# Performance work log

Hardware: AMD Instinct MI355X
Metric: run time of the kernel (lower is better)

## Reference

```python
import jax, jax.numpy as jnp
import numpy as np

N_ENTITY = 100000
H_DIM = 512
N_ROWS = 262144
ALPHA = 0.5          # EMA rate for fast state
GATE_TH = 0.5        # gate_threshold buffer
GATE_SCALE = 5.0     # gate_scale buffer
LN_EPS = 1e-5


def setup_inputs() -> dict:
    key = jax.random.key(0)
    k1, k2, k3, k4, k5 = jax.random.split(key, 5)
    entity_emb = jax.random.normal(k1, (N_ROWS, H_DIM), dtype=jnp.float32)
    entity_ids = jax.random.randint(k2, (N_ROWS,), 0, N_ENTITY, dtype=jnp.int64)
    slow_state = 0.1 * jax.random.normal(k3, (N_ENTITY, H_DIM), dtype=jnp.float32)
    fast_state = 0.1 * jax.random.normal(k4, (N_ENTITY, H_DIM), dtype=jnp.float32)
    # torch nn.Linear(2h, h): weight shape (h, 2h), y = x @ W.T + b
    W = jax.random.normal(k5, (H_DIM, 2 * H_DIM), dtype=jnp.float32) * 0.02
    b = jnp.zeros((H_DIM,), dtype=jnp.float32)
    return {"entity_emb": entity_emb, "slow_state": slow_state,
            "fast_state": fast_state, "W": W, "b": b, "entity_ids": entity_ids}


def _layer_norm(x):
    mu = jnp.mean(x, axis=-1, keepdims=True)
    var = jnp.mean(jnp.square(x - mu), axis=-1, keepdims=True)
    return (x - mu) * jax.lax.rsqrt(var + LN_EPS)


def reference(entity_emb, slow_state, fast_state, W, b, entity_ids):
    # ---- fuse_with_state (gate path) ----
    state = slow_state[entity_ids]                                   # (N, h) gather
    is_active = (jnp.sum(jnp.abs(state), axis=-1, keepdims=True) > 1e-6).astype(entity_emb.dtype)
    h_state = _layer_norm(state)
    gate_in = jnp.concatenate([entity_emb, h_state], axis=-1)        # (N, 2h)
    z = jax.nn.sigmoid(gate_in @ W.T + b)                            # (N, h)
    fused = z * entity_emb + (1.0 - z) * h_state
    out = is_active * fused + (1.0 - is_active) * entity_emb

    # ---- writeback (no-grad in torch; scatter-reduce EMA + norm-gated slow update) ----
    ctx = jax.lax.stop_gradient(out)
    ids = entity_ids
    counts = jax.ops.segment_sum(jnp.ones((ctx.shape[0],), ctx.dtype), ids,
                                 num_segments=N_ENTITY)              # (E,)
    ctx_sum = jax.ops.segment_sum(ctx, ids, num_segments=N_ENTITY)   # (E, h)
    ctx_mean = ctx_sum / jnp.clip(counts, 1.0)[:, None]
    touched = (counts > 0)[:, None]
    new_fast_all = (1.0 - ALPHA) * fast_state + ALPHA * ctx_mean
    new_fast = jnp.where(touched, new_fast_all, fast_state)
    diff = new_fast - slow_state
    delta = jnp.linalg.norm(diff, axis=-1, keepdims=True)
    gate = jax.nn.sigmoid(GATE_SCALE * (delta - GATE_TH))
    new_slow = jnp.where(touched, slow_state + gate * diff, slow_state)
    return out, new_fast, new_slow
```

## Files before the change

### kernel.cpp

```cpp
#include <hip/hip_runtime.h>
#include <hip/hip_bf16.h>
#include <cstdint>

#define NROWS 262144
#define HDIM  512
#define NENT  100000
#define SCAN_NBLK ((NENT + 1023) / 1024)

typedef __attribute__((ext_vector_type(4))) float  f32x4;
typedef __attribute__((ext_vector_type(8))) short  bf16x8;
typedef __attribute__((ext_vector_type(4))) short  bf16x4;

static __device__ __forceinline__ unsigned short f2bf(float x) {
    unsigned u = __float_as_uint(x);
    u += 0x7FFF + ((u >> 16) & 1);
    return (unsigned short)(u >> 16);
}
static __device__ __forceinline__ float bf2f(unsigned short h) {
    return __uint_as_float(((unsigned)h) << 16);
}

__global__ void pack_w_kernel(const float* __restrict__ W,
                              unsigned short* __restrict__ WeP,
                              unsigned short* __restrict__ WsP) {
    int g    = blockIdx.x * 256 + threadIdx.x;
    int sel  = g >> 15;
    int gg   = g & 32767;
    int lane = gg & 63;
    int kt   = (gg >> 6) & 15;
    int nt   = gg >> 10;
    int col  = nt * 16 + (lane & 15);
    int k    = kt * 32 + ((lane >> 4) << 3) + sel * 512;
    const float* src = W + (size_t)col * 1024 + k;
    f32x4 v0 = *(const f32x4*)(src);
    f32x4 v1 = *(const f32x4*)(src + 4);
    bf16x8 ov;
#pragma unroll
    for (int i = 0; i < 4; ++i) {
        ov[i]     = (short)f2bf(v0[i]);
        ov[4 + i] = (short)f2bf(v1[i]);
    }
    unsigned short* dst = sel ? WsP : WeP;
    *(bf16x8*)(dst + (size_t)gg * 8) = ov;
}

__global__ __launch_bounds__(256) void zero_kernel(unsigned* __restrict__ p) {
    int i = blockIdx.x * 256 + threadIdx.x;
    if (i < NENT) p[i] = 0u;
}

__global__ __launch_bounds__(256) void count_kernel(const int* __restrict__ ids,
                                                    unsigned* __restrict__ counts) {
    int r = blockIdx.x * 256 + threadIdx.x;
    if (r < NROWS) atomicAdd(&counts[ids[r]], 1u);
}

__global__ __launch_bounds__(1024) void scan1_kernel(const unsigned* __restrict__ counts,
                                                     unsigned* __restrict__ off,
                                                     unsigned* __restrict__ bsums) {
    __shared__ unsigned tmp[1024];
    int i = blockIdx.x * 1024 + threadIdx.x;
    unsigned v = (i < NENT) ? counts[i] : 0u;
    tmp[threadIdx.x] = v;
    __syncthreads();
#pragma unroll
    for (int o = 1; o < 1024; o <<= 1) {
        unsigned a = (threadIdx.x >= o) ? tmp[threadIdx.x - o] : 0u;
        __syncthreads();
        tmp[threadIdx.x] += a;
        __syncthreads();
    }
    if (i < NENT) off[i] = tmp[threadIdx.x] - v;
    if (threadIdx.x == 1023) bsums[blockIdx.x] = tmp[1023];
}

__global__ void scan2_kernel(unsigned* __restrict__ bsums) {
    if (threadIdx.x == 0 && blockIdx.x == 0) {
        unsigned s = 0;
        for (int i = 0; i < SCAN_NBLK; ++i) { unsigned t = bsums[i]; bsums[i] = s; s += t; }
    }
}

__global__ __launch_bounds__(1024) void scan3_kernel(unsigned* __restrict__ off,
                                                     const unsigned* __restrict__ bsums,
                                                     unsigned* __restrict__ cursor) {
    int i = blockIdx.x * 1024 + threadIdx.x;
    if (i < NENT) {
        unsigned o = off[i] + bsums[blockIdx.x];
        off[i] = o;
        cursor[i] = o;
    }
    if (i == 0) off[NENT] = NROWS;
}

__global__ __launch_bounds__(256) void fill_kernel(const int* __restrict__ ids,
                                                   unsigned* __restrict__ cursor,
                                                   int* __restrict__ rowidx) {
    int r = blockIdx.x * 256 + threadIdx.x;
    if (r < NROWS) {
        unsigned p = atomicAdd(&cursor[ids[r]], 1u);
        rowidx[p] = r;
    }
}

__global__ __launch_bounds__(512, 4) void entity_kernel(
    const float* __restrict__ slow, const unsigned short* __restrict__ WsP,
    const float* __restrict__ bias, unsigned short* __restrict__ hB,
    unsigned short* __restrict__ GsB, float* __restrict__ actB)
{
    __shared__ unsigned short xLds[2048 * 8];
    __shared__ float muS[32], rsS[32], bS[512];

    const int t    = threadIdx.x;
    const int w    = t >> 6;
    const int lane = t & 63;
    const int brow = blockIdx.x * 32;

    if (t < 128) ((f32x4*)bS)[t] = ((const f32x4*)bias)[t];

    for (int rr = 0; rr < 4; ++rr) {
        int row = w * 4 + rr;
        int e   = brow + row;
        const float* sp = slow + (size_t)e * HDIM;
        f32x4 v0 = ((const f32x4*)sp)[lane * 2];
        f32x4 v1 = ((const f32x4*)sp)[lane * 2 + 1];
        float s = 0.f, s2 = 0.f, sa = 0.f;
#pragma unroll
        for (int i = 0; i < 4; ++i) {
            s  += v0[i] + v1[i];
            s2 += v0[i] * v0[i] + v1[i] * v1[i];
            sa += fabsf(v0[i]) + fabsf(v1[i]);
        }
#pragma unroll
        for (int m = 32; m >= 1; m >>= 1) {
            s  += __shfl_xor(s, m);
            s2 += __shfl_xor(s2, m);
            sa += __shfl_xor(sa, m);
        }
        if (lane == 0) {
            float mu  = s * (1.f / HDIM);
            float var = s2 * (1.f / HDIM) - mu * mu;
            muS[row] = mu;
            rsS[row] = rsqrtf(var + 1e-5f);
            actB[e]  = (sa > 1e-6f) ? 1.f : 0.f;
        }
    }
    __syncthreads();

#pragma unroll
    for (int i = 0; i < 4; ++i) {
        int s  = t + i * 512;
        int T  = s >> 6, ls = s & 63;
        int row = (T & 1) * 16 + (ls & 15);
        int k   = (T >> 1) * 32 + ((ls >> 4) << 3);
        const float* p = slow + (size_t)(brow + row) * HDIM + k;
        f32x4 x0 = *(const f32x4*)p, x1 = *(const f32x4*)(p + 4);
        float mu = muS[row], rs = rsS[row];
        bf16x8 av;
#pragma unroll
        for (int j = 0; j < 4; ++j) {
            av[j]     = (short)f2bf((x0[j] - mu) * rs);
            av[4 + j] = (short)f2bf((x1[j] - mu) * rs);
        }
        ((bf16x8*)xLds)[s] = av;
    }
    __syncthreads();

    f32x4 zero4 = {0.f, 0.f, 0.f, 0.f};
    f32x4 acc[2][4];
#pragma unroll
    for (int i = 0; i < 2; ++i)
#pragma unroll
        for (int j = 0; j < 4; ++j) acc[i][j] = zero4;

#define LOADW_A(dst, kt)                                                \
    {   _Pragma("unroll")                                               \
        for (int ct = 0; ct < 4; ++ct)                                  \
            dst[ct] = *(const bf16x8*)(WsP +                            \
                ((size_t)(((w * 4 + ct) * 16 + (kt)) * 64 + lane) << 3)); \
    }
#define LOADX_A(dst, kt)                                                \
    {   _Pragma("unroll")                                               \
        for (int rt = 0; rt < 2; ++rt)                                  \
            dst[rt] = ((const bf16x8*)xLds)[((kt) * 2 + rt) * 64 + lane]; \
    }
#define STEP(wf, xf)                                                    \
    {   _Pragma("unroll")                                               \
        for (int ct = 0; ct < 4; ++ct) {                                \
            acc[0][ct] = __builtin_amdgcn_mfma_f32_16x16x32_bf16(wf[ct], xf[0], acc[0][ct], 0, 0, 0); \
            acc[1][ct] = __builtin_amdgcn_mfma_f32_16x16x32_bf16(wf[ct], xf[1], acc[1][ct], 0, 0, 0); \
        }                                                               \
    }

    {
        bf16x8 wA[4], wB[4], xA[2], xB[2];
        LOADW_A(wA, 0); LOADX_A(xA, 0);
#pragma unroll
        for (int kt = 0; kt < 16; kt += 2) {
            if (kt + 1 < 16) { LOADW_A(wB, kt + 1); LOADX_A(xB, kt + 1); }
            STEP(wA, xA);
            if (kt + 2 < 16) { LOADW_A(wA, kt + 2); LOADX_A(xA, kt + 2); }
            if (kt + 1 < 16) STEP(wB, xB);
        }
    }
#undef LOADW_A
#undef LOADX_A

#pragma unroll
    for (int rt = 0; rt < 2; ++rt) {
        int e = brow + rt * 16 + (lane & 15);
#pragma unroll
        for (int ct = 0; ct < 4; ++ct) {
            int col0 = w * 64 + ct * 16 + ((lane >> 4) << 2);
            f32x4 bv = *(const f32x4*)&bS[col0];
            bf16x4 gv;
#pragma unroll
            for (int r = 0; r < 4; ++r) gv[r] = (short)f2bf(acc[rt][ct][r] + bv[r]);
            *(bf16x4*)(GsB + (size_t)e * HDIM + col0) = gv;
        }
    }
#pragma unroll
    for (int i = 0; i < 4; ++i) {
        int s  = t + i * 512;
        int T  = s >> 6, ls = s & 63;
        int row = (T & 1) * 16 + (ls & 15);
        int k   = (T >> 1) * 32 + ((ls >> 4) << 3);
        *(bf16x8*)(hB + (size_t)(brow + row) * HDIM + k) = ((const bf16x8*)xLds)[s];
    }
}

__global__ __launch_bounds__(1024, 4) void fuse_kernel(
    const float* __restrict__ emb, const unsigned short* __restrict__ WeP,
    const int* __restrict__ ids, const unsigned short* __restrict__ hB,
    const unsigned short* __restrict__ GsB, const float* __restrict__ actB,
    float* __restrict__ out)
{
    __shared__ unsigned short xLds[4096 * 8];
    __shared__ int idS[64];

    const int t    = threadIdx.x;
    const int w    = t >> 6;
    const int lane = t & 63;
    const int wm   = w >> 3;
    const int wn   = w & 7;
    const int brow = blockIdx.x * 64;

    if (t < 64) idS[t] = ids[brow + t];

#pragma unroll
    for (int i = 0; i < 4; ++i) {
        int s  = t + i * 1024;
        int T  = s >> 6, ls = s & 63;
        int kt  = T >> 2, rt = T & 3;
        int row = rt * 16 + (ls & 15);
        int k   = kt * 32 + ((ls >> 4) << 3);
        const float* p = emb + (size_t)(brow + row) * HDIM + k;
        f32x4 x0 = *(const f32x4*)p, x1 = *(const f32x4*)(p + 4);
        bf16x8 av;
#pragma unroll
        for (int j = 0; j < 4; ++j) {
            av[j]     = (short)f2bf(x0[j]);
            av[4 + j] = (short)f2bf(x1[j]);
        }
        ((bf16x8*)xLds)[s] = av;
    }
    __syncthreads();

    f32x4 zero4 = {0.f, 0.f, 0.f, 0.f};
    f32x4 acc[2][4];
#pragma unroll
    for (int i = 0; i < 2; ++i)
#pragma unroll
        for (int j = 0; j < 4; ++j) acc[i][j] = zero4;

#define LOADW_B(dst, kt)                                                \
    {   _Pragma("unroll")                                               \
        for (int ct = 0; ct < 4; ++ct)                                  \
            dst[ct] = *(const bf16x8*)(WeP +                            \
                ((size_t)(((wn * 4 + ct) * 16 + (kt)) * 64 + lane) << 3)); \
    }
#define LOADX_B(dst, kt)                                                \
    {   _Pragma("unroll")                                               \
        for (int rt = 0; rt < 2; ++rt)                                  \
            dst[rt] = ((const bf16x8*)xLds)[((kt) * 4 + wm * 2 + rt) * 64 + lane]; \
    }

    {
        bf16x8 wA[4], wB[4], xA[2], xB[2];
        LOADW_B(wA, 0); LOADX_B(xA, 0);
#pragma unroll
        for (int kt = 0; kt < 16; kt += 2) {
            if (kt + 1 < 16) { LOADW_B(wB, kt + 1); LOADX_B(xB, kt + 1); }
            STEP(wA, xA);
            if (kt + 2 < 16) { LOADW_B(wA, kt + 2); LOADX_B(xA, kt + 2); }
            if (kt + 1 < 16) STEP(wB, xB);
        }
    }
#undef LOADW_B
#undef LOADX_B
#undef STEP

#pragma unroll
    for (int rt = 0; rt < 2; ++rt) {
        int rowl = wm * 32 + rt * 16 + (lane & 15);
        int grow = brow + rowl;
        int id   = idS[rowl];
        float act = actB[id];
        const unsigned short* gsP = GsB + (size_t)id * HDIM;
        const unsigned short* hP  = hB  + (size_t)id * HDIM;
        float* outP = out + (size_t)grow * HDIM;
#pragma unroll
        for (int ct = 0; ct < 4; ++ct) {
            int col0 = wn * 64 + ct * 16 + ((lane >> 4) << 2);
            int Te = ((col0 >> 5) * 4 + wm * 2 + rt) * 64 + (((col0 >> 3) & 3) << 4) + (lane & 15);
            const unsigned short* pe = xLds + Te * 8 + (col0 & 7);
            bf16x4 gv = *(const bf16x4*)(gsP + col0);
            bf16x4 hv = *(const bf16x4*)(hP + col0);
            f32x4 o;
#pragma unroll
            for (int r = 0; r < 4; ++r) {
                float ev = bf2f(pe[r]);
                float logit = acc[rt][ct][r] + bf2f(gv[r]);
                float z = 1.f / (1.f + __expf(-logit));
                float fused = z * ev + (1.f - z) * bf2f(hv[r]);
                o[r] = (act > 0.f) ? fused : ev;
            }
            *(f32x4*)(outP + col0) = o;
        }
    }
}

__global__ __launch_bounds__(256) void finalize_kernel(
    const float* __restrict__ fast, const float* __restrict__ slow,
    const float* __restrict__ out, const unsigned* __restrict__ off,
    const int* __restrict__ rowidx, float* __restrict__ nf, float* __restrict__ ns)
{
    int e = blockIdx.x * 4 + (threadIdx.x >> 6);
    if (e >= NENT) return;
    int lane = threadIdx.x & 63;
    size_t base = (size_t)e * HDIM + lane * 8;

    f32x4 f0 = *(const f32x4*)(fast + base), f1 = *(const f32x4*)(fast + base + 4);
    f32x4 l0 = *(const f32x4*)(slow + base), l1 = *(const f32x4*)(slow + base + 4);

    unsigned o0 = off[e], o1 = off[e + 1];
    int c = (int)(o1 - o0);

    if (c == 0) {
        *(f32x4*)(nf + base)     = f0;
        *(f32x4*)(nf + base + 4) = f1;
        *(f32x4*)(ns + base)     = l0;
        *(f32x4*)(ns + base + 4) = l1;
        return;
    }

    f32x4 s0 = {0.f, 0.f, 0.f, 0.f}, s1 = {0.f, 0.f, 0.f, 0.f};
    for (int j = 0; j < c; ++j) {
        int r = rowidx[o0 + j];
        const float* p = out + (size_t)r * HDIM + lane * 8;
        s0 += *(const f32x4*)p;
        s1 += *(const f32x4*)(p + 4);
    }

    float inv = 0.5f / (float)c;
    f32x4 n0, n1, d0, d1;
    float ss = 0.f;
#pragma unroll
    for (int i = 0; i < 4; ++i) {
        n0[i] = 0.5f * f0[i] + s0[i] * inv;
        n1[i] = 0.5f * f1[i] + s1[i] * inv;
        d0[i] = n0[i] - l0[i]; ss += d0[i] * d0[i];
        d1[i] = n1[i] - l1[i]; ss += d1[i] * d1[i];
    }
#pragma unroll
    for (int m = 32; m >= 1; m >>= 1) ss += __shfl_xor(ss, m);
    float delta = sqrtf(ss);
    float gate  = 1.f / (1.f + expf(-5.f * (delta - 0.5f)));

    f32x4 o0v, o1v;
#pragma unroll
    for (int i = 0; i < 4; ++i) {
        o0v[i] = l0[i] + gate * d0[i];
        o1v[i] = l1[i] + gate * d1[i];
    }
    *(f32x4*)(nf + base)     = n0;
    *(f32x4*)(nf + base + 4) = n1;
    *(f32x4*)(ns + base)     = o0v;
    *(f32x4*)(ns + base + 4) = o1v;
}

extern "C" void kernel_launch(void* const* d_in, const int* in_sizes, int n_in,
                              void* d_out, int out_size, void* d_ws, size_t ws_size,
                              hipStream_t stream) {
    const float* emb  = (const float*)d_in[0];
    const float* slow = (const float*)d_in[1];
    const float* fast = (const float*)d_in[2];
    const float* W    = (const float*)d_in[3];
    const float* bias = (const float*)d_in[4];
    const int*   ids  = (const int*)d_in[5];

    float* out = (float*)d_out;
    float* nf  = out + (size_t)NROWS * HDIM;
    float* ns  = nf + (size_t)NENT * HDIM;

    unsigned short* hB  = (unsigned short*)nf;
    unsigned short* GsB = (unsigned short*)ns;

    unsigned short* WeP = (unsigned short*)d_ws;
    unsigned short* WsP = (unsigned short*)((char*)d_ws + (512u << 10));
    float* actB         = (float*)((char*)d_ws + (1024u << 10));
    unsigned* counts    = (unsigned*)((char*)d_ws + (1536u << 10));
    unsigned* off       = (unsigned*)((char*)d_ws + (2048u << 10));
    unsigned* bsums     = (unsigned*)((char*)d_ws + (2560u << 10));
    int*      rowidx    = (int*)((char*)d_ws + (2560u << 10) + 4096);

    zero_kernel<<<(NENT + 255) / 256, 256, 0, stream>>>(counts);
    pack_w_kernel<<<256, 256, 0, stream>>>(W, WeP, WsP);
    entity_kernel<<<NENT / 32, 512, 0, stream>>>(slow, WsP, bias, hB, GsB, actB);
    count_kernel<<<NROWS / 256, 256, 0, stream>>>(ids, counts);
    scan1_kernel<<<SCAN_NBLK, 1024, 0, stream>>>(counts, off, bsums);
    scan2_kernel<<<1, 64, 0, stream>>>(bsums);
    scan3_kernel<<<SCAN_NBLK, 1024, 0, stream>>>(off, bsums, counts);
    fill_kernel<<<NROWS / 256, 256, 0, stream>>>(ids, counts, rowidx);
    fuse_kernel<<<NROWS / 64, 1024, 0, stream>>>(emb, WeP, ids, hB, GsB, actB, out);
    finalize_kernel<<<(NENT + 3) / 4, 256, 0, stream>>>(fast, slow, out, off, rowidx, nf, ns);
}
```

Before: 974.6 us.

## Merge setup kernels, fold counting into entity kernel, split fuse staging, unroll gather

Merges the weight-pack and count-zeroing kernels into one launch and moves the per-row id counting atomics into entity_kernel, removing two kernel launches. In fuse_kernel, the second half of the embedding tile is loaded into registers while the first half of the K loop runs, then packed into shared memory before the second half. The finalize gather loop is unrolled by four to issue more independent row loads. The changes save launch overhead and hide some memory latency, at the cost of more register pressure and an extra barrier in the fuse kernel.

```diff
diff --git a/kernel.cpp b/kernel.cpp
--- a/kernel.cpp
+++ b/kernel.cpp
@@ -20,39 +20,35 @@
     return __uint_as_float(((unsigned)h) << 16);
 }
 
-__global__ void pack_w_kernel(const float* __restrict__ W,
-                              unsigned short* __restrict__ WeP,
-                              unsigned short* __restrict__ WsP) {
-    int g    = blockIdx.x * 256 + threadIdx.x;
-    int sel  = g >> 15;
-    int gg   = g & 32767;
-    int lane = gg & 63;
-    int kt   = (gg >> 6) & 15;
-    int nt   = gg >> 10;
-    int col  = nt * 16 + (lane & 15);
-    int k    = kt * 32 + ((lane >> 4) << 3) + sel * 512;
-    const float* src = W + (size_t)col * 1024 + k;
-    f32x4 v0 = *(const f32x4*)(src);
-    f32x4 v1 = *(const f32x4*)(src + 4);
-    bf16x8 ov;
-#pragma unroll
-    for (int i = 0; i < 4; ++i) {
-        ov[i]     = (short)f2bf(v0[i]);
-        ov[4 + i] = (short)f2bf(v1[i]);
-    }
-    unsigned short* dst = sel ? WsP : WeP;
-    *(bf16x8*)(dst + (size_t)gg * 8) = ov;
-}
-
-__global__ __launch_bounds__(256) void zero_kernel(unsigned* __restrict__ p) {
-    int i = blockIdx.x * 256 + threadIdx.x;
-    if (i < NENT) p[i] = 0u;
-}
-
-__global__ __launch_bounds__(256) void count_kernel(const int* __restrict__ ids,
-                                                    unsigned* __restrict__ counts) {
-    int r = blockIdx.x * 256 + threadIdx.x;
-    if (r < NROWS) atomicAdd(&counts[ids[r]], 1u);
+__global__ __launch_bounds__(256) void pack_zero_kernel(
+    const float* __restrict__ W, unsigned short* __restrict__ WeP,
+    unsigned short* __restrict__ WsP, unsigned* __restrict__ counts)
+{
+    int bid = blockIdx.x;
+    if (bid < 256) {
+        int g    = bid * 256 + threadIdx.x;
+        int sel  = g >> 15;
+        int gg   = g & 32767;
+        int lane = gg & 63;
+        int kt   = (gg >> 6) & 15;
+        int nt   = gg >> 10;
+        int col  = nt * 16 + (lane & 15);
+        int k    = kt * 32 + ((lane >> 4) << 3) + sel * 512;
+        const float* src = W + (size_t)col * 1024 + k;
+        f32x4 v0 = *(const f32x4*)(src);
+        f32x4 v1 = *(const f32x4*)(src + 4);
+        bf16x8 ov;
+#pragma unroll
+        for (int i = 0; i < 4; ++i) {
+            ov[i]     = (short)f2bf(v0[i]);
+            ov[4 + i] = (short)f2bf(v1[i]);
+        }
+        unsigned short* dst = sel ? WsP : WeP;
+        *(bf16x8*)(dst + (size_t)gg * 8) = ov;
+    } else {
+        int i = (bid - 256) * 256 + threadIdx.x;
+        if (i < NENT) counts[i] = 0u;
+    }
 }
 
 __global__ __launch_bounds__(1024) void scan1_kernel(const unsigned* __restrict__ counts,
@@ -105,7 +101,8 @@
 
 __global__ __launch_bounds__(512, 4) void entity_kernel(
     const float* __restrict__ slow, const unsigned short* __restrict__ WsP,
-    const float* __restrict__ bias, unsigned short* __restrict__ hB,
+    const float* __restrict__ bias, const int* __restrict__ ids,
+    unsigned* __restrict__ counts, unsigned short* __restrict__ hB,
     unsigned short* __restrict__ GsB, float* __restrict__ actB)
 {
     __shared__ unsigned short xLds[2048 * 8];
@@ -115,6 +112,11 @@
     const int w    = t >> 6;
     const int lane = t & 63;
     const int brow = blockIdx.x * 32;
+
+    {
+        int gid = blockIdx.x * 512 + t;
+        if (gid < NROWS) atomicAdd(&counts[ids[gid]], 1u);
+    }
 
     if (t < 128) ((f32x4*)bS)[t] = ((const f32x4*)bias)[t];
 
@@ -247,24 +249,41 @@
 
     if (t < 64) idS[t] = ids[brow + t];
 
-#pragma unroll
-    for (int i = 0; i < 4; ++i) {
-        int s  = t + i * 1024;
-        int T  = s >> 6, ls = s & 63;
-        int kt  = T >> 2, rt = T & 3;
-        int row = rt * 16 + (ls & 15);
-        int k   = kt * 32 + ((ls >> 4) << 3);
+#define XGEO(s, row, k)                                                  \
+    int T_ = (s) >> 6, ls_ = (s) & 63;                                   \
+    row = (T_ & 3) * 16 + (ls_ & 15);                                    \
+    k   = (T_ >> 2) * 32 + ((ls_ >> 4) << 3);
+
+#define XPACK(s, x0, x1)                                                 \
+    {   bf16x8 av_;                                                      \
+        _Pragma("unroll")                                                \
+        for (int j = 0; j < 4; ++j) {                                    \
+            av_[j]     = (short)f2bf(x0[j]);                             \
+            av_[4 + j] = (short)f2bf(x1[j]);                             \
+        }                                                                \
+        ((bf16x8*)xLds)[s] = av_;                                        \
+    }
+
+#pragma unroll
+    for (int i = 0; i < 2; ++i) {
+        int s = t + i * 1024;
+        int row, k; XGEO(s, row, k);
         const float* p = emb + (size_t)(brow + row) * HDIM + k;
         f32x4 x0 = *(const f32x4*)p, x1 = *(const f32x4*)(p + 4);
-        bf16x8 av;
-#pragma unroll
-        for (int j = 0; j < 4; ++j) {
-            av[j]     = (short)f2bf(x0[j]);
-            av[4 + j] = (short)f2bf(x1[j]);
-        }
-        ((bf16x8*)xLds)[s] = av;
+        XPACK(s, x0, x1);
     }
     __syncthreads();
+
+    f32x4 h20, h21, h30, h31;
+    int row2, k2, row3, k3;
+    { int s = t + 2048; XGEO(s, row2, k2); }
+    { int s = t + 3072; XGEO(s, row3, k3); }
+    {
+        const float* p2 = emb + (size_t)(brow + row2) * HDIM + k2;
+        const float* p3 = emb + (size_t)(brow + row3) * HDIM + k3;
+        h20 = *(const f32x4*)p2; h21 = *(const f32x4*)(p2 + 4);
+        h30 = *(const f32x4*)p3; h31 = *(const f32x4*)(p3 + 4);
+    }
 
     f32x4 zero4 = {0.f, 0.f, 0.f, 0.f};
     f32x4 acc[2][4];
@@ -289,16 +308,34 @@
         bf16x8 wA[4], wB[4], xA[2], xB[2];
         LOADW_B(wA, 0); LOADX_B(xA, 0);
 #pragma unroll
-        for (int kt = 0; kt < 16; kt += 2) {
-            if (kt + 1 < 16) { LOADW_B(wB, kt + 1); LOADX_B(xB, kt + 1); }
+        for (int kt = 0; kt < 8; kt += 2) {
+            LOADW_B(wB, kt + 1); LOADX_B(xB, kt + 1);
+            STEP(wA, xA);
+            if (kt + 2 < 8) { LOADW_B(wA, kt + 2); LOADX_B(xA, kt + 2); }
+            STEP(wB, xB);
+        }
+    }
+
+    XPACK(t + 2048, h20, h21);
+    XPACK(t + 3072, h30, h31);
+    __syncthreads();
+
+    {
+        bf16x8 wA[4], wB[4], xA[2], xB[2];
+        LOADW_B(wA, 8); LOADX_B(xA, 8);
+#pragma unroll
+        for (int kt = 8; kt < 16; kt += 2) {
+            LOADW_B(wB, kt + 1); LOADX_B(xB, kt + 1);
             STEP(wA, xA);
             if (kt + 2 < 16) { LOADW_B(wA, kt + 2); LOADX_B(xA, kt + 2); }
-            if (kt + 1 < 16) STEP(wB, xB);
+            STEP(wB, xB);
         }
     }
 #undef LOADW_B
 #undef LOADX_B
 #undef STEP
+#undef XGEO
+#undef XPACK
 
 #pragma unroll
     for (int rt = 0; rt < 2; ++rt) {
@@ -355,8 +392,23 @@
     }
 
     f32x4 s0 = {0.f, 0.f, 0.f, 0.f}, s1 = {0.f, 0.f, 0.f, 0.f};
-    for (int j = 0; j < c; ++j) {
-        int r = rowidx[o0 + j];
+    int j = (int)o0, end = (int)o1;
+    while (j + 4 <= end) {
+        int r0 = rowidx[j], r1 = rowidx[j + 1], r2 = rowidx[j + 2], r3 = rowidx[j + 3];
+        const float* p0 = out + (size_t)r0 * HDIM + lane * 8;
+        const float* p1 = out + (size_t)r1 * HDIM + lane * 8;
+        const float* p2 = out + (size_t)r2 * HDIM + lane * 8;
+        const float* p3 = out + (size_t)r3 * HDIM + lane * 8;
+        f32x4 a0 = *(const f32x4*)p0, b0 = *(const f32x4*)(p0 + 4);
+        f32x4 a1 = *(const f32x4*)p1, b1 = *(const f32x4*)(p1 + 4);
+        f32x4 a2 = *(const f32x4*)p2, b2 = *(const f32x4*)(p2 + 4);
+        f32x4 a3 = *(const f32x4*)p3, b3 = *(const f32x4*)(p3 + 4);
+        s0 += a0 + a1 + a2 + a3;
+        s1 += b0 + b1 + b2 + b3;
+        j += 4;
+    }
+    while (j < end) {
+        int r = rowidx[j++];
         const float* p = out + (size_t)r * HDIM + lane * 8;
         s0 += *(const f32x4*)p;
         s1 += *(const f32x4*)(p + 4);
@@ -414,10 +466,8 @@
     unsigned* bsums     = (unsigned*)((char*)d_ws + (2560u << 10));
     int*      rowidx    = (int*)((char*)d_ws + (2560u << 10) + 4096);
 
-    zero_kernel<<<(NENT + 255) / 256, 256, 0, stream>>>(counts);
-    pack_w_kernel<<<256, 256, 0, stream>>>(W, WeP, WsP);
-    entity_kernel<<<NENT / 32, 512, 0, stream>>>(slow, WsP, bias, hB, GsB, actB);
-    count_kernel<<<NROWS / 256, 256, 0, stream>>>(ids, counts);
+    pack_zero_kernel<<<256 + (NENT + 255) / 256, 256, 0, stream>>>(W, WeP, WsP, counts);
+    entity_kernel<<<NENT / 32, 512, 0, stream>>>(slow, WsP, bias, ids, counts, hB, GsB, actB);
     scan1_kernel<<<SCAN_NBLK, 1024, 0, stream>>>(counts, off, bsums);
     scan2_kernel<<<1, 64, 0, stream>>>(bsums);
     scan3_kernel<<<SCAN_NBLK, 1024, 0, stream>>>(off, bsums, counts);
```

Result: slower. 997.4 us (+2.3%).
